# Performance work log

Hardware: AMD Instinct MI355X
Metric: run time of the kernel (lower is better)

## Reference

```python
import jax, jax.numpy as jnp
import numpy as np

B, N, D = 8, 1024, 768
H = 12
HD = D // H  # 64
SCALE = HD ** (-0.5)


def setup_inputs() -> dict:
    key = jax.random.key(0)
    ks = jax.random.split(key, 11)
    s = 0.02
    return {
        "x": jax.random.normal(ks[0], (B, N, D), dtype=jnp.float32),
        "w_q": jax.random.normal(ks[1], (D, D), dtype=jnp.float32) * s,
        "b_q": jax.random.normal(ks[2], (D,), dtype=jnp.float32) * s,
        "w_k": jax.random.normal(ks[3], (D, D), dtype=jnp.float32) * s,
        "b_k": jax.random.normal(ks[4], (D,), dtype=jnp.float32) * s,
        "w_v": jax.random.normal(ks[5], (D, D), dtype=jnp.float32) * s,
        "b_v": jax.random.normal(ks[6], (D,), dtype=jnp.float32) * s,
        "w_qt": jax.random.normal(ks[7], (D, D), dtype=jnp.float32) * s,
        "b_qt": jax.random.normal(ks[8], (D,), dtype=jnp.float32) * s,
        "w_p": jax.random.normal(ks[9], (D, D), dtype=jnp.float32) * s,
        "b_p": jax.random.normal(ks[10], (D,), dtype=jnp.float32) * s,
    }


def _heads(y):
    # [B,N,D] -> [B,H,N,HD]
    b, n, d = y.shape
    return y.reshape(b, n, H, HD).transpose(0, 2, 1, 3)


def reference(x, w_q, b_q, w_k, b_k, w_v, b_v, w_qt, b_qt, w_p, b_p):
    # torch nn.Linear: y = x @ W.T + b
    q = _heads(x @ w_q.T + b_q)
    k = _heads(x @ w_k.T + b_k)
    v = _heads(x @ w_v.T + b_v)
    q_tilde = _heads(x @ w_qt.T + b_qt)
    # NOTE: source divides by self.scale = head_dim**-0.5 (i.e. multiplies by sqrt(hd)); reproduced faithfully
    corr = jnp.einsum("bhnd,bhmd->bhnm", q_tilde, k) / SCALE
    scores = jnp.einsum("bhnd,bhmd->bhnm", q, k) / SCALE + corr
    attn = jax.nn.softmax(scores, axis=-1)
    out = jnp.einsum("bhnm,bhmd->bhnd", attn, v)  # [B,H,N,HD]
    out = out.transpose(0, 2, 1, 3).reshape(x.shape[0], x.shape[1], D)
    out = out @ w_p.T + b_p
    return out, corr
```

## Files before the change

kernel.cpp:

```cpp
#include <hip/hip_runtime.h>

typedef __bf16 bf16_t;
typedef __bf16 bf16x8 __attribute__((ext_vector_type(8)));
typedef __bf16 bf16x4 __attribute__((ext_vector_type(4)));
typedef float f32x4 __attribute__((ext_vector_type(4)));

constexpr int BATCH = 8;
constexpr int NSEQ = 1024;
constexpr int DMODEL = 768;
constexpr int NH = 12;
constexpr int HDIM = 64;
constexpr int MROWS = BATCH * NSEQ;
constexpr int WSZ = DMODEL * DMODEL;
constexpr float L2E = 1.44269504088896f;

#define AS1(p) ((const __attribute__((address_space(1))) void*)(p))
#define AS3(p) ((__attribute__((address_space(3))) void*)(p))

__global__ __launch_bounds__(256) void prep_w(
    const float* __restrict__ wq, const float* __restrict__ wqt,
    const float* __restrict__ wk, const float* __restrict__ wv,
    const float* __restrict__ wp, const float* __restrict__ bq,
    const float* __restrict__ bqt, ushort* __restrict__ wb_,
    float* __restrict__ bqs, float* __restrict__ bqt8)
{
    int i = blockIdx.x * 256 + threadIdx.x;
    bf16_t* w = (bf16_t*)wb_;
    float a = wq[i], b = wqt[i];
    w[i]            = (bf16_t)(8.0f * (a + b));
    w[WSZ + i]      = (bf16_t)(8.0f * b);
    w[2*WSZ + i]    = (bf16_t)wk[i];
    w[3*WSZ + i]    = (bf16_t)wv[i];
    w[4*WSZ + i]    = (bf16_t)wp[i];
    if (i < DMODEL) {
        bqs[i]  = 8.0f * (bq[i] + bqt[i]);
        bqt8[i] = 8.0f * bqt[i];
    }
}

__global__ __launch_bounds__(256) void conv_x(const float* __restrict__ x,
                                              ushort* __restrict__ xb_)
{
    int i = (blockIdx.x * 256 + threadIdx.x) * 4;
    float4 v = *(const float4*)(x + i);
    bf16x4 r = { (bf16_t)v.x, (bf16_t)v.y, (bf16_t)v.z, (bf16_t)v.w };
    *(bf16x4*)((bf16_t*)xb_ + i) = r;
}

__device__ __forceinline__ void gemm_core(
    const bf16_t* __restrict__ A, const bf16_t* __restrict__ W,
    bf16_t* As, bf16_t* Bs, int m0, int n0, int tid, f32x4 acc[4][4])
{
    const int lane = tid & 63, wave = tid >> 6;
    const int g = lane >> 4, c = lane & 15;
    const int wm = wave >> 1, wn = wave & 1;

    const int r_b = tid >> 3;
    const int koff = 8 * ((tid & 7) ^ (r_b & 7));
    const size_t arow = (size_t)(m0 + r_b) * DMODEL + koff;
    const size_t brow = (size_t)(n0 + r_b) * DMODEL + koff;
    char* As_base = (char*)As + (tid & ~63) * 16;
    char* Bs_base = (char*)Bs + (tid & ~63) * 16;

    for (int k0 = 0; k0 < DMODEL; k0 += 64) {
        __syncthreads();
#pragma unroll
        for (int i = 0; i < 4; i++)
            __builtin_amdgcn_global_load_lds(
                AS1(A + arow + k0 + (size_t)i * 32 * DMODEL),
                AS3(As_base + i * 4096), 16, 0, 0);
#pragma unroll
        for (int i = 0; i < 4; i++)
            __builtin_amdgcn_global_load_lds(
                AS1(W + brow + k0 + (size_t)i * 32 * DMODEL),
                AS3(Bs_base + i * 4096), 16, 0, 0);
        __syncthreads();
#pragma unroll
        for (int kk = 0; kk < 2; kk++) {
            bf16x8 af[4], bfr[4];
#pragma unroll
            for (int mt = 0; mt < 4; mt++) {
                int r = wm * 64 + mt * 16 + c;
                af[mt] = *(const bf16x8*)(As + r * 64 + ((kk * 4 + g) ^ (r & 7)) * 8);
            }
#pragma unroll
            for (int nt = 0; nt < 4; nt++) {
                int r = wn * 64 + nt * 16 + c;
                bfr[nt] = *(const bf16x8*)(Bs + r * 64 + ((kk * 4 + g) ^ (r & 7)) * 8);
            }
#pragma unroll
            for (int mt = 0; mt < 4; mt++)
#pragma unroll
                for (int nt = 0; nt < 4; nt++)
                    acc[mt][nt] = __builtin_amdgcn_mfma_f32_16x16x32_bf16(
                        af[mt], bfr[nt], acc[mt][nt], 0, 0, 0);
        }
    }
}

__global__ __launch_bounds__(256) void gemm_qkv(
    const ushort* __restrict__ xb_, const ushort* __restrict__ wb_,
    const float* __restrict__ bqs, const float* __restrict__ bqt8,
    const float* __restrict__ bk, const float* __restrict__ bv,
    ushort* __restrict__ o0, ushort* __restrict__ o1,
    ushort* __restrict__ o2, ushort* __restrict__ o3)
{
    __shared__ alignas(16) bf16_t As[128 * 64];
    __shared__ alignas(16) bf16_t Bs[128 * 64];
    const int bid = blockIdx.x;
    const int gid = (bid & 7) * 192 + (bid >> 3);
    const int z = gid / 384;
    const int rr = gid % 384;
    const int m0 = (rr / 6) * 128, n0 = (rr % 6) * 128;

    const bf16_t* A = (const bf16_t*)xb_;
    const bf16_t* W = (const bf16_t*)wb_ + (size_t)z * WSZ;
    const float* bias = (z == 0) ? bqs : (z == 1) ? bqt8 : (z == 2) ? bk : bv;
    bf16_t* outp = (bf16_t*)((z == 0) ? o0 : (z == 1) ? o1 : (z == 2) ? o2 : o3);
    f32x4 acc[4][4] = {};
    gemm_core(A, W, As, Bs, m0, n0, threadIdx.x, acc);

    const int tid = threadIdx.x, lane = tid & 63, wave = tid >> 6;
    const int g = lane >> 4, c = lane & 15;
    const int wm = wave >> 1, wn = wave & 1;
#pragma unroll
    for (int mt = 0; mt < 4; mt++)
#pragma unroll
        for (int nt = 0; nt < 4; nt++) {
            int col = n0 + wn * 64 + nt * 16 + c;
            int h = col >> 6, hd = col & 63;
            float bsv = bias[col];
            if (z == 3) {
                int row0 = m0 + wm * 64 + mt * 16 + 4 * g;
                int b = row0 >> 10, ns0 = row0 & 1023;
                bf16x4 pb = { (bf16_t)(acc[mt][nt][0] + bsv),
                              (bf16_t)(acc[mt][nt][1] + bsv),
                              (bf16_t)(acc[mt][nt][2] + bsv),
                              (bf16_t)(acc[mt][nt][3] + bsv) };
                *(bf16x4*)(outp + ((size_t)(b * NH + h) * HDIM + hd) * NSEQ + ns0) = pb;
            } else {
#pragma unroll
                for (int j = 0; j < 4; j++) {
                    int row = m0 + wm * 64 + mt * 16 + 4 * g + j;
                    int b = row >> 10, ns = row & 1023;
                    outp[(((size_t)b * NH + h) * NSEQ + ns) * HDIM + hd] =
                        (bf16_t)(acc[mt][nt][j] + bsv);
                }
            }
        }
}

__global__ __launch_bounds__(256) void gemm_out(
    const ushort* __restrict__ ao_, const ushort* __restrict__ wp_,
    const float* __restrict__ bp, float* __restrict__ out)
{
    __shared__ alignas(16) bf16_t As[128 * 64];
    __shared__ alignas(16) bf16_t Bs[128 * 64];
    const int bid = blockIdx.x;
    const int gid = (bid & 7) * 48 + (bid >> 3);
    const int m0 = (gid / 6) * 128, n0 = (gid % 6) * 128;

    const bf16_t* A = (const bf16_t*)ao_;
    const bf16_t* W = (const bf16_t*)wp_;
    f32x4 acc[4][4] = {};
    gemm_core(A, W, As, Bs, m0, n0, threadIdx.x, acc);

    const int tid = threadIdx.x, lane = tid & 63, wave = tid >> 6;
    const int g = lane >> 4, c = lane & 15;
    const int wm = wave >> 1, wn = wave & 1;
#pragma unroll
    for (int mt = 0; mt < 4; mt++)
#pragma unroll
        for (int nt = 0; nt < 4; nt++) {
            int col = n0 + wn * 64 + nt * 16 + c;
            float bsv = bp[col];
#pragma unroll
            for (int j = 0; j < 4; j++) {
                int row = m0 + wm * 64 + mt * 16 + 4 * g + j;
                out[(size_t)row * DMODEL + col] = acc[mt][nt][j] + bsv;
            }
        }
}

__global__ __launch_bounds__(256, 2) void attn_kernel(
    const ushort* __restrict__ qs_, const ushort* __restrict__ qt_,
    const ushort* __restrict__ kb_, const ushort* __restrict__ vt_,
    ushort* __restrict__ ao_, float* __restrict__ corr)
{
    __shared__ alignas(16) bf16_t VT[2][64 * 64];
    __shared__ alignas(16) bf16_t P[4][32 * 72];
    const bf16_t* QS = (const bf16_t*)qs_;
    const bf16_t* QT = (const bf16_t*)qt_;
    const bf16_t* Kb = (const bf16_t*)kb_;
    const bf16_t* Vt = (const bf16_t*)vt_;
    bf16_t* Ob = (bf16_t*)ao_;

    const int tid = threadIdx.x;
    const int w = tid >> 6, lane = tid & 63;
    const int g = lane >> 4, c = lane & 15;
    const int bid = blockIdx.x;
    const int gid = (bid & 7) * 96 + (bid >> 3);
    const int bh = gid >> 3, qb = gid & 7;
    const int q00 = qb * 128 + w * 32;
    const size_t base = (size_t)bh * (NSEQ * HDIM);

    bf16x8 qsf[2][2], qtf[2][2];
#pragma unroll
    for (int s = 0; s < 2; s++)
#pragma unroll
        for (int kk = 0; kk < 2; kk++) {
            const size_t qrow = base + (size_t)(q00 + s * 16 + c) * HDIM + kk * 32 + 8 * g;
            qsf[s][kk] = *(const bf16x8*)(QS + qrow);
            qtf[s][kk] = *(const bf16x8*)(QT + qrow);
        }
    f32x4 oacc[2][4] = {};
    float mrun[2], lrun[2];
#pragma unroll
    for (int s = 0; s < 2; s++) { mrun[s] = -3e30f; lrun[s] = 0.f; }

    float* corr_b = corr + (size_t)bh * (NSEQ * NSEQ);

    const int hd0_ = tid >> 3, ch0_ = tid & 7;
    const int hd1_ = hd0_ + 32;

    for (int t = 0; t < 16; t++) {
        const int kv0 = t * 64;
        bf16_t* vt = VT[t & 1];
        {
            bf16x8 v0 = *(const bf16x8*)(Vt + base + (size_t)hd0_ * NSEQ + kv0 + ch0_ * 8);
            bf16x8 v1 = *(const bf16x8*)(Vt + base + (size_t)hd1_ * NSEQ + kv0 + ch0_ * 8);
            *(bf16x8*)(vt + hd0_ * 64 + ((ch0_ ^ (hd0_ & 7)) * 8)) = v0;
            *(bf16x8*)(vt + hd1_ * 64 + ((ch0_ ^ (hd1_ & 7)) * 8)) = v1;
        }
        bf16x8 kf[4][2];
#pragma unroll
        for (int kvt = 0; kvt < 4; kvt++) {
            const size_t krow = base + (size_t)(kv0 + kvt * 16 + c) * HDIM + 8 * g;
            kf[kvt][0] = *(const bf16x8*)(Kb + krow);
            kf[kvt][1] = *(const bf16x8*)(Kb + krow + 32);
        }
        f32x4 sv[2][4];
#pragma unroll
        for (int kvt = 0; kvt < 4; kvt++) {
#pragma unroll
            for (int s = 0; s < 2; s++) {
                f32x4 sa = {0.f, 0.f, 0.f, 0.f};
                f32x4 ca = {0.f, 0.f, 0.f, 0.f};
                sa = __builtin_amdgcn_mfma_f32_16x16x32_bf16(kf[kvt][0], qsf[s][0], sa, 0, 0, 0);
                sa = __builtin_amdgcn_mfma_f32_16x16x32_bf16(kf[kvt][1], qsf[s][1], sa, 0, 0, 0);
                ca = __builtin_amdgcn_mfma_f32_16x16x32_bf16(kf[kvt][0], qtf[s][0], ca, 0, 0, 0);
                ca = __builtin_amdgcn_mfma_f32_16x16x32_bf16(kf[kvt][1], qtf[s][1], ca, 0, 0, 0);
                sv[s][kvt] = sa;
                *(f32x4*)(corr_b + (size_t)(q00 + s * 16 + c) * NSEQ + kv0 + kvt * 16 + 4 * g) = ca;
            }
        }
#pragma unroll
        for (int s = 0; s < 2; s++) {
            f32x4 mm;
#pragma unroll
            for (int j = 0; j < 4; j++)
                mm[j] = fmaxf(fmaxf(sv[s][0][j], sv[s][1][j]),
                              fmaxf(sv[s][2][j], sv[s][3][j]));
            float tm = fmaxf(fmaxf(mm[0], mm[1]), fmaxf(mm[2], mm[3]));
            tm = fmaxf(tm, __shfl_xor(tm, 16));
            tm = fmaxf(tm, __shfl_xor(tm, 32));
            if (__any(tm > mrun[s] + 8.0f)) {
                float newm = fmaxf(mrun[s], tm);
                float scl = exp2f((mrun[s] - newm) * L2E);
                mrun[s] = newm;
                lrun[s] *= scl;
#pragma unroll
                for (int j = 0; j < 4; j++) {
                    float scj = __shfl(scl, 4 * g + j);
#pragma unroll
                    for (int nt = 0; nt < 4; nt++) oacc[s][nt][j] *= scj;
                }
            }
            const float mneg = mrun[s] * L2E;
            float ps = 0.f;
#pragma unroll
            for (int kvt = 0; kvt < 4; kvt++)
#pragma unroll
                for (int j = 0; j < 4; j++) {
                    float p = exp2f(__builtin_fmaf(sv[s][kvt][j], L2E, -mneg));
                    sv[s][kvt][j] = p;
                    ps += p;
                }
            ps += __shfl_xor(ps, 16);
            ps += __shfl_xor(ps, 32);
            lrun[s] += ps;
#pragma unroll
            for (int kvt = 0; kvt < 4; kvt++) {
                bf16x4 pb = { (bf16_t)sv[s][kvt][0], (bf16_t)sv[s][kvt][1],
                              (bf16_t)sv[s][kvt][2], (bf16_t)sv[s][kvt][3] };
                *(bf16x4*)(&P[w][(s * 16 + c) * 72 + kvt * 16 + 4 * g]) = pb;
            }
        }
        asm volatile("s_waitcnt lgkmcnt(0)" ::: "memory");
        __builtin_amdgcn_sched_barrier(0);
        __builtin_amdgcn_s_barrier();
#pragma unroll
        for (int kk = 0; kk < 2; kk++) {
#pragma unroll
            for (int nt = 0; nt < 4; nt++) {
                const int hd = nt * 16 + c;
                bf16x8 vf = *(const bf16x8*)(&vt[hd * 64 + (((kk * 4 + g) ^ (hd & 7)) * 8)]);
#pragma unroll
                for (int s = 0; s < 2; s++) {
                    bf16x8 pa = *(const bf16x8*)(&P[w][(s * 16 + c) * 72 + kk * 32 + 8 * g]);
                    oacc[s][nt] = __builtin_amdgcn_mfma_f32_16x16x32_bf16(pa, vf, oacc[s][nt], 0, 0, 0);
                }
            }
        }
    }
    const int b = bh / NH, h = bh % NH;
#pragma unroll
    for (int s = 0; s < 2; s++) {
        float lj[4];
#pragma unroll
        for (int j = 0; j < 4; j++) lj[j] = __shfl(lrun[s], 4 * g + j);
#pragma unroll
        for (int nt = 0; nt < 4; nt++)
#pragma unroll
            for (int j = 0; j < 4; j++) {
                float val = oacc[s][nt][j] / lj[j];
                Ob[(size_t)(b * NSEQ + q00 + s * 16 + 4 * g + j) * DMODEL + h * HDIM + nt * 16 + c] =
                    (bf16_t)val;
            }
    }
}

extern "C" void kernel_launch(void* const* d_in, const int* in_sizes, int n_in,
                              void* d_out, int out_size, void* d_ws, size_t ws_size,
                              hipStream_t stream)
{
    const float* x   = (const float*)d_in[0];
    const float* wq  = (const float*)d_in[1];
    const float* bq  = (const float*)d_in[2];
    const float* wk  = (const float*)d_in[3];
    const float* bk  = (const float*)d_in[4];
    const float* wv  = (const float*)d_in[5];
    const float* bv  = (const float*)d_in[6];
    const float* wqt = (const float*)d_in[7];
    const float* bqt = (const float*)d_in[8];
    const float* wp  = (const float*)d_in[9];
    const float* bp  = (const float*)d_in[10];

    char* ws = (char*)d_ws;
    ushort* xb   = (ushort*)(ws);
    ushort* wb   = (ushort*)(ws + 12582912);
    float*  bqs  = (float*)(ws + 18481152);
    float*  bqt8 = (float*)(ws + 18485248);
    ushort* qs   = (ushort*)(ws + 18489344);
    ushort* qt   = qs + 6291456;
    ushort* kb   = qt + 6291456;
    ushort* vt   = kb + 6291456;
    ushort* ao   = vt + 6291456;

    float* out  = (float*)d_out;
    float* corr = out + (size_t)6291456;

    prep_w<<<2304, 256, 0, stream>>>(wq, wqt, wk, wv, wp, bq, bqt, wb, bqs, bqt8);
    conv_x<<<6144, 256, 0, stream>>>(x, xb);
    gemm_qkv<<<1536, 256, 0, stream>>>(xb, wb, bqs, bqt8, bk, bv, qs, qt, kb, vt);
    attn_kernel<<<768, 256, 0, stream>>>(qs, qt, kb, vt, ao, corr);
    gemm_out<<<384, 256, 0, stream>>>(ao, wb + (size_t)4 * WSZ, bp, out);
}
```

Before: 248.3 us.

## Software-pipeline K and V tile loads one iteration ahead in attention loop

Prefetches the next tile's V rows into registers at the start of each iteration and the next K fragments after the softmax, then writes V into the alternate LDS buffer after the PV MMAs. The barrier moves to the end of the iteration. The aim is to hide global load latency behind the QK/softmax/PV compute. In exchange it raises register pressure, which could lower occupancy. P is written to LDS and read by the same wave without an intervening barrier; this is fine if P is per-wave.

```diff
diff --git a/kernel.cpp b/kernel.cpp
--- a/kernel.cpp
+++ b/kernel.cpp
@@ -222,22 +222,32 @@
 
     const int hd0_ = tid >> 3, ch0_ = tid & 7;
     const int hd1_ = hd0_ + 32;
+    const int vtoff0 = hd0_ * 64 + (ch0_ ^ (hd0_ & 7)) * 8;
+    const int vtoff1 = hd1_ * 64 + (ch0_ ^ (hd1_ & 7)) * 8;
+
+    bf16x8 vrA = *(const bf16x8*)(Vt + base + (size_t)hd0_ * NSEQ + ch0_ * 8);
+    bf16x8 vrB = *(const bf16x8*)(Vt + base + (size_t)hd1_ * NSEQ + ch0_ * 8);
+    bf16x8 kf[4][2];
+#pragma unroll
+    for (int kvt = 0; kvt < 4; kvt++) {
+        const size_t krow = base + (size_t)(kvt * 16 + c) * HDIM + 8 * g;
+        kf[kvt][0] = *(const bf16x8*)(Kb + krow);
+        kf[kvt][1] = *(const bf16x8*)(Kb + krow + 32);
+    }
+    *(bf16x8*)(VT[0] + vtoff0) = vrA;
+    *(bf16x8*)(VT[0] + vtoff1) = vrB;
+    asm volatile("s_waitcnt lgkmcnt(0)" ::: "memory");
+    __builtin_amdgcn_sched_barrier(0);
+    __builtin_amdgcn_s_barrier();
 
     for (int t = 0; t < 16; t++) {
         const int kv0 = t * 64;
-        bf16_t* vt = VT[t & 1];
-        {
-            bf16x8 v0 = *(const bf16x8*)(Vt + base + (size_t)hd0_ * NSEQ + kv0 + ch0_ * 8);
-            bf16x8 v1 = *(const bf16x8*)(Vt + base + (size_t)hd1_ * NSEQ + kv0 + ch0_ * 8);
-            *(bf16x8*)(vt + hd0_ * 64 + ((ch0_ ^ (hd0_ & 7)) * 8)) = v0;
-            *(bf16x8*)(vt + hd1_ * 64 + ((ch0_ ^ (hd1_ & 7)) * 8)) = v1;
-        }
-        bf16x8 kf[4][2];
-#pragma unroll
-        for (int kvt = 0; kvt < 4; kvt++) {
-            const size_t krow = base + (size_t)(kv0 + kvt * 16 + c) * HDIM + 8 * g;
-            kf[kvt][0] = *(const bf16x8*)(Kb + krow);
-            kf[kvt][1] = *(const bf16x8*)(Kb + krow + 32);
+        const int kvn = kv0 + 64;
+        bf16_t* vtc = VT[t & 1];
+        bf16_t* vtn = VT[(t + 1) & 1];
+        if (t < 15) {
+            vrA = *(const bf16x8*)(Vt + base + (size_t)hd0_ * NSEQ + kvn + ch0_ * 8);
+            vrB = *(const bf16x8*)(Vt + base + (size_t)hd1_ * NSEQ + kvn + ch0_ * 8);
         }
         f32x4 sv[2][4];
 #pragma unroll
@@ -296,15 +306,20 @@
                 *(bf16x4*)(&P[w][(s * 16 + c) * 72 + kvt * 16 + 4 * g]) = pb;
             }
         }
-        asm volatile("s_waitcnt lgkmcnt(0)" ::: "memory");
-        __builtin_amdgcn_sched_barrier(0);
-        __builtin_amdgcn_s_barrier();
+        if (t < 15) {
+#pragma unroll
+            for (int kvt = 0; kvt < 4; kvt++) {
+                const size_t krow = base + (size_t)(kvn + kvt * 16 + c) * HDIM + 8 * g;
+                kf[kvt][0] = *(const bf16x8*)(Kb + krow);
+                kf[kvt][1] = *(const bf16x8*)(Kb + krow + 32);
+            }
+        }
 #pragma unroll
         for (int kk = 0; kk < 2; kk++) {
 #pragma unroll
             for (int nt = 0; nt < 4; nt++) {
                 const int hd = nt * 16 + c;
-                bf16x8 vf = *(const bf16x8*)(&vt[hd * 64 + (((kk * 4 + g) ^ (hd & 7)) * 8)]);
+                bf16x8 vf = *(const bf16x8*)(&vtc[hd * 64 + (((kk * 4 + g) ^ (hd & 7)) * 8)]);
 #pragma unroll
                 for (int s = 0; s < 2; s++) {
                     bf16x8 pa = *(const bf16x8*)(&P[w][(s * 16 + c) * 72 + kk * 32 + 8 * g]);
@@ -312,6 +327,13 @@
                 }
             }
         }
+        if (t < 15) {
+            *(bf16x8*)(vtn + vtoff0) = vrA;
+            *(bf16x8*)(vtn + vtoff1) = vrB;
+        }
+        asm volatile("s_waitcnt lgkmcnt(0)" ::: "memory");
+        __builtin_amdgcn_sched_barrier(0);
+        __builtin_amdgcn_s_barrier();
     }
     const int b = bh / NH, h = bh % NH;
 #pragma unroll
```

After: 224.5 us. 1.11x faster.
